# Optimization experiments

Measured on AMD Instinct MI355X. Metric: run time of the kernel, lower is better.

## Reference

```python
import jax, jax.numpy as jnp
import numpy as np

B, S, D, H, E = 4, 1024, 1024, 16, 4
HD = D // H
EPS = 1e-5


def setup_inputs() -> dict:
    key = jax.random.key(0)
    ks = jax.random.split(key, 6)
    std = 0.02
    return {
        "hidden_states": jax.random.normal(ks[0], (B, S, D), dtype=jnp.float32),
        "Wr": jax.random.normal(ks[1], (D, E), dtype=jnp.float32) * std,
        "br": jnp.zeros((E,), jnp.float32),
        "ln_g": jnp.ones((E, D), jnp.float32),
        "ln_b": jnp.zeros((E, D), jnp.float32),
        "W_attn": jax.random.normal(ks[2], (E, D, 3 * D), dtype=jnp.float32) * std,
        "b_attn": jnp.zeros((E, 3 * D), jnp.float32),
        "W_proj": jax.random.normal(ks[3], (E, D, D), dtype=jnp.float32) * std,
        "b_proj": jnp.zeros((E, D), jnp.float32),
    }


def reference(hidden_states, Wr, br, ln_g, ln_b, W_attn, b_attn, W_proj, b_proj):
    b, s, d = hidden_states.shape
    x = hidden_states.reshape(b * s, d)  # [N, D]

    # naive softmax router over experts
    score = jax.nn.softmax(x @ Wr + br, axis=-1)  # [N, E]

    # LayerNorm stats are expert-independent; affine is per-expert
    mu = jnp.mean(x, axis=-1, keepdims=True)
    var = jnp.mean(jnp.square(x - mu), axis=-1, keepdims=True)
    xn = (x - mu) * jax.lax.rsqrt(var + EPS)  # [N, D]

    ln_out = xn[:, None, :] * ln_g[None] + ln_b[None]  # [N, E, D]
    qkv_all = jnp.einsum('ned,edf->nef', ln_out, W_attn) + b_attn  # [N, E, 3D]
    # weighted_qkv: scale each expert's qkv by its routing score, sum
    qkv = jnp.einsum('ne,nef->nf', score, qkv_all)  # [N, 3D]

    q, k, v = jnp.split(qkv.reshape(b, s, 3 * d), 3, axis=-1)
    def split_heads(t):
        return t.reshape(b, s, H, HD).transpose(0, 2, 1, 3)  # [B,H,S,hd]
    q, k, v = split_heads(q), split_heads(k), split_heads(v)

    scale = 1.0 / jnp.sqrt(jnp.asarray(HD, q.dtype))
    att = jnp.einsum('bhqd,bhkd->bhqk', q, k) * scale  # [B,H,S,S]
    causal = jnp.tril(jnp.ones((s, s), dtype=bool))
    att = jnp.where(causal[None, None], att, jnp.finfo(att.dtype).min)
    probs = jax.nn.softmax(att, axis=-1)
    ctx = jnp.einsum('bhqk,bhkd->bhqd', probs, v)  # [B,H,S,hd]
    ctx = ctx.transpose(0, 2, 1, 3).reshape(b * s, d)  # [N, D]

    proj_all = jnp.einsum('nd,edf->nef', ctx, W_proj) + b_proj  # [N, E, D]
    out = jnp.einsum('ne,nef->nf', score, proj_all).reshape(b, s, d)
    return out
```

## Files before the change

### kernel.cpp

```cpp
#include <hip/hip_runtime.h>
#include <stdint.h>

#define NB 4
#define SS 1024
#define DD 1024
#define EE 4
#define HH 16
#define HDD 64
#define NN (NB*SS)
#define KK2 (EE*DD)
#define FF1 (3*DD)

typedef __attribute__((ext_vector_type(4))) float f32x4;
typedef __attribute__((ext_vector_type(8))) _Float16 half8;
typedef __attribute__((ext_vector_type(4))) _Float16 half4;

static __device__ __forceinline__ f32x4 mfma16(half8 a, half8 b, f32x4 c){
  return __builtin_amdgcn_mfma_f32_16x16x32_f16(a, b, c, 0, 0, 0);
}

#define GLOAD_LDS16(gp, lp) __builtin_amdgcn_global_load_lds( \
    (const unsigned int __attribute__((address_space(1)))*)(uintptr_t)(gp), \
    (unsigned int __attribute__((address_space(3)))*)(uintptr_t)(lp), 16, 0, 0)

#define SBAR() do { asm volatile("" ::: "memory"); \
                    __builtin_amdgcn_s_barrier(); \
                    asm volatile("" ::: "memory"); } while(0)

__device__ __forceinline__ void prep_body(
    const float* __restrict__ x, const float* __restrict__ Wr,
    const float* __restrict__ br, float* __restrict__ score,
    float* __restrict__ ratios, _Float16* __restrict__ xnb,
    int n, float (*red)[6])
{
  int tid = threadIdx.x;
  float4 xv = ((const float4*)(x + (size_t)n*DD))[tid];
  float xa[4] = {xv.x, xv.y, xv.z, xv.w};
  float vals[6];
  vals[0] = xa[0]+xa[1]+xa[2]+xa[3];
  vals[1] = xa[0]*xa[0]+xa[1]*xa[1]+xa[2]*xa[2]+xa[3]*xa[3];
  vals[2] = vals[3] = vals[4] = vals[5] = 0.f;
  #pragma unroll
  for (int j = 0; j < 4; ++j){
    float4 w = ((const float4*)Wr)[tid*4 + j];
    vals[2] += xa[j]*w.x; vals[3] += xa[j]*w.y;
    vals[4] += xa[j]*w.z; vals[5] += xa[j]*w.w;
  }
  #pragma unroll
  for (int off = 32; off >= 1; off >>= 1)
    #pragma unroll
    for (int i = 0; i < 6; ++i)
      vals[i] += __shfl_xor(vals[i], off, 64);
  int wid = tid >> 6;
  if ((tid & 63) == 0){
    #pragma unroll
    for (int i = 0; i < 6; ++i) red[wid][i] = vals[i];
  }
  __syncthreads();
  float tot[6];
  #pragma unroll
  for (int i = 0; i < 6; ++i)
    tot[i] = red[0][i] + red[1][i] + red[2][i] + red[3][i];

  float mu   = tot[0] * (1.f/DD);
  float var  = tot[1] * (1.f/DD) - mu*mu;
  float rsig = rsqrtf(var + 1e-5f);
  float lg[4];
  #pragma unroll
  for (int e = 0; e < 4; ++e) lg[e] = tot[2+e] + br[e];
  float mx = fmaxf(fmaxf(lg[0], lg[1]), fmaxf(lg[2], lg[3]));
  float ex[4], esum = 0.f;
  #pragma unroll
  for (int e = 0; e < 4; ++e){ ex[e] = __expf(lg[e] - mx); esum += ex[e]; }
  if (tid < 4){
    score[n*4 + tid] = ex[tid] / esum;
    ratios[n*4 + tid] = (tid > 0) ? (ex[tid-1] / ex[tid]) : 0.f;
  }

  half4 o;
  #pragma unroll
  for (int j = 0; j < 4; ++j) o[j] = (_Float16)((xa[j] - mu) * rsig);
  *(half4*)(xnb + (size_t)n*DD + tid*4) = o;
}

template<bool AFFINE>
__device__ __forceinline__ void transpose_body(
    const float* __restrict__ W, _Float16* __restrict__ WT, int K, int F,
    const float* __restrict__ gvec, const float* __restrict__ bvec,
    float* __restrict__ part, int k0, int f0,
    float (*t)[65], float (*red2)[64])
{
  int tid = threadIdx.x;
  int r = tid >> 4, c4 = (tid & 15) * 4;
  float pf[4] = {0.f, 0.f, 0.f, 0.f};
  #pragma unroll
  for (int i = 0; i < 4; ++i){
    int k = k0 + i*16 + r;
    float4 v = *(const float4*)(W + (size_t)k*F + f0 + c4);
    if constexpr (AFFINE){
      float bk = bvec[k];
      pf[0] += bk*v.x; pf[1] += bk*v.y; pf[2] += bk*v.z; pf[3] += bk*v.w;
      float gk = gvec[k];
      v.x *= gk; v.y *= gk; v.z *= gk; v.w *= gk;
    }
    t[i*16 + r][c4+0] = v.x; t[i*16 + r][c4+1] = v.y;
    t[i*16 + r][c4+2] = v.z; t[i*16 + r][c4+3] = v.w;
  }
  if constexpr (AFFINE){
    #pragma unroll
    for (int j = 0; j < 4; ++j) red2[r][c4+j] = pf[j];
  }
  __syncthreads();
  int f = tid >> 2, seg = tid & 3;
  half8 o0, o1;
  #pragma unroll
  for (int j = 0; j < 8; ++j){
    o0[j] = (_Float16)t[seg*16 + j][f];
    o1[j] = (_Float16)t[seg*16 + 8 + j][f];
  }
  _Float16* dst = WT + (size_t)(f0 + f)*K + k0 + seg*16;
  *(half8*)dst = o0;
  *(half8*)(dst + 8) = o1;
  if constexpr (AFFINE){
    if (tid < 64){
      float s = 0.f;
      #pragma unroll
      for (int rr = 0; rr < 16; ++rr) s += red2[rr][tid];
      part[(size_t)(k0/64) * F + f0 + tid] = s;
    }
  }
}

__global__ __launch_bounds__(256) void prep_fused_kernel(
    const float* __restrict__ W1, _Float16* __restrict__ W1T,
    const float* __restrict__ W2, _Float16* __restrict__ W2T,
    const float* __restrict__ gvec, const float* __restrict__ bvec,
    float* __restrict__ part,
    const float* __restrict__ x, const float* __restrict__ Wr,
    const float* __restrict__ br, float* __restrict__ score,
    float* __restrict__ ratios, _Float16* __restrict__ xnb)
{
  __shared__ float t[64][65];
  __shared__ float red2[16][64];
  __shared__ float red[4][6];
  int id = blockIdx.x;
  if (id & 1){
    prep_body(x, Wr, br, score, ratios, xnb, id >> 1, red);
  } else {
    int tr = id >> 1;
    int k0 = (tr & 63) * 64;
    int y  = tr >> 6;
    if (y < FF1/64)
      transpose_body<true >(W1, W1T, KK2, FF1, gvec, bvec, part, k0, y*64, t, red2);
    else
      transpose_body<false>(W2, W2T, KK2, DD, nullptr, nullptr, nullptr,
                            k0, (y - FF1/64)*64, t, red2);
  }
}

__global__ __launch_bounds__(256) void bb1_kernel(
    const float* __restrict__ b_attn, const float* __restrict__ part,
    float* __restrict__ BB1)
{
  int idx = blockIdx.x*256 + threadIdx.x;
  int e = idx / FF1, f = idx - e*FF1;
  float s = b_attn[idx];
  #pragma unroll
  for (int i = 0; i < 16; ++i)
    s += part[(size_t)(e*16 + i)*FF1 + f];
  BB1[idx] = s;
}

#define G1_BM 256
#define G1_BN 192
#define G1_BK 64
#define G1_T  (KK2/G1_BK)
#define G1_ABUF (G1_BM*G1_BK)
#define G1_BBUF (G1_BN*G1_BK)
#define G1_BUFSZ (G1_ABUF+G1_BBUF)

__global__ __launch_bounds__(512, 2) void gemm1_kernel(
    const _Float16* __restrict__ XN, const _Float16* __restrict__ BT,
    const float* __restrict__ score, const float* __restrict__ ratios,
    const float* __restrict__ bias, _Float16* __restrict__ C)
{
  __shared__ _Float16 smem[2*G1_BUFSZ];
  int tid = threadIdx.x;
  int lane = tid & 63, wid = tid >> 6;
  int q = lane & 15, g = lane >> 4;
  int wr = wid >> 1, wc = wid & 1;
  int xo = (q & 7) << 3;
  int bid = blockIdx.x;
  int xcd = bid & 7, li = bid >> 3;
  int m0 = (li >> 1) * G1_BM;
  int n0 = (xcd*2 + (li & 1)) * G1_BN;

  int arow[4], brow[6];
  #pragma unroll
  for (int mf = 0; mf < 4; ++mf) arow[mf] = (wr*64 + mf*16 + q)*64;
  #pragma unroll
  for (int nf = 0; nf < 6; ++nf) brow[nf] = G1_ABUF + (wc*96 + nf*16 + q)*64;
  int soff[2] = { (g*8) ^ xo, (32 + g*8) ^ xo };

  auto stageA = [&](int t, int buf, int h){
    const int d0 = (t & 15) * G1_BK;
    _Float16* sA = smem + buf*G1_BUFSZ;
    #pragma unroll
    for (int ld = 0; ld < 2; ++ld){
      int l = h*2 + ld;
      int c = l*512 + tid;
      int row = c >> 3;
      int seg = (c & 7) ^ (row & 7);
      GLOAD_LDS16(XN + (size_t)(m0 + row)*DD + d0 + seg*8,
                  sA + (l*512 + wid*64)*8);
    }
  };
  auto stageB = [&](int t, int buf){
    const int k0 = t * G1_BK;
    _Float16* sB = smem + buf*G1_BUFSZ + G1_ABUF;
    #pragma unroll
    for (int ld = 0; ld < 3; ++ld){
      int c = ld*512 + tid;
      int row = c >> 3;
      int seg = (c & 7) ^ (row & 7);
      GLOAD_LDS16(BT + (size_t)(n0 + row)*KK2 + k0 + seg*8,
                  sB + (ld*512 + wid*64)*8);
    }
  };

  f32x4 acc[4][6] = {};
  half8 af0[2][2], af2[2][2], bf[6][2];

  stageA(0, 0, 0); stageA(0, 0, 1); stageB(0, 0);

  for (int t = 0; t < G1_T-1; ++t){
    if (t && (t & 15) == 0){
      int e = t >> 4;
      #pragma unroll
      for (int mf = 0; mf < 4; ++mf)
        #pragma unroll
        for (int r = 0; r < 4; ++r){
          int gm = m0 + wr*64 + mf*16 + g*4 + r;
          float ratio = ratios[gm*4 + e];
          #pragma unroll
          for (int nf = 0; nf < 6; ++nf)
            acc[mf][nf][r] *= ratio;
        }
    }
    int buf = t & 1, nxt = buf ^ 1;
    const _Float16* base = smem + buf*G1_BUFSZ;
    stageA(t+1, nxt, 0);
    asm volatile("s_waitcnt vmcnt(2)" ::: "memory");
    SBAR();
    #pragma unroll
    for (int m = 0; m < 2; ++m)
      #pragma unroll
      for (int k = 0; k < 2; ++k)
        af0[m][k] = *(const half8*)(base + arow[m] + soff[k]);
    #pragma unroll
    for (int n = 0; n < 3; ++n)
      #pragma unroll
      for (int k = 0; k < 2; ++k)
        bf[n][k] = *(const half8*)(base + brow[n] + soff[k]);
    stageA(t+1, nxt, 1);
    __builtin_amdgcn_s_setprio(1);
    #pragma unroll
    for (int k = 0; k < 2; ++k)
      #pragma unroll
      for (int m = 0; m < 2; ++m)
        #pragma unroll
        for (int n = 0; n < 3; ++n)
          acc[m][n] = mfma16(af0[m][k], bf[n][k], acc[m][n]);
    __builtin_amdgcn_s_setprio(0);
    #pragma unroll
    for (int n = 3; n < 6; ++n)
      #pragma unroll
      for (int k = 0; k < 2; ++k)
        bf[n][k] = *(const half8*)(base + brow[n] + soff[k]);
    stageB(t+1, nxt);
    SBAR();
    __builtin_amdgcn_s_setprio(1);
    #pragma unroll
    for (int k = 0; k < 2; ++k)
      #pragma unroll
      for (int m = 0; m < 2; ++m)
        #pragma unroll
        for (int n = 3; n < 6; ++n)
          acc[m][n] = mfma16(af0[m][k], bf[n][k], acc[m][n]);
    __builtin_amdgcn_s_setprio(0);
    #pragma unroll
    for (int m = 0; m < 2; ++m)
      #pragma unroll
      for (int k = 0; k < 2; ++k)
        af2[m][k] = *(const half8*)(base + arow[2+m] + soff[k]);
    SBAR();
    __builtin_amdgcn_s_setprio(1);
    #pragma unroll
    for (int k = 0; k < 2; ++k)
      #pragma unroll
      for (int m = 0; m < 2; ++m)
        #pragma unroll
        for (int n = 3; n < 6; ++n)
          acc[2+m][n] = mfma16(af2[m][k], bf[n][k], acc[2+m][n]);
    #pragma unroll
    for (int k = 0; k < 2; ++k)
      #pragma unroll
      for (int m = 0; m < 2; ++m)
        #pragma unroll
        for (int n = 0; n < 3; ++n)
          acc[2+m][n] = mfma16(af2[m][k], bf[n][k], acc[2+m][n]);
    __builtin_amdgcn_s_setprio(0);
  }
  {
    const _Float16* base = smem + ((G1_T-1) & 1)*G1_BUFSZ;
    asm volatile("s_waitcnt vmcnt(0)" ::: "memory");
    SBAR();
    #pragma unroll
    for (int m = 0; m < 2; ++m)
      #pragma unroll
      for (int k = 0; k < 2; ++k){
        af0[m][k] = *(const half8*)(base + arow[m] + soff[k]);
        af2[m][k] = *(const half8*)(base + arow[2+m] + soff[k]);
      }
    #pragma unroll
    for (int n = 0; n < 6; ++n)
      #pragma unroll
      for (int k = 0; k < 2; ++k)
        bf[n][k] = *(const half8*)(base + brow[n] + soff[k]);
    #pragma unroll
    for (int k = 0; k < 2; ++k)
      #pragma unroll
      for (int m = 0; m < 2; ++m)
        #pragma unroll
        for (int n = 0; n < 6; ++n){
          acc[m][n]   = mfma16(af0[m][k], bf[n][k], acc[m][n]);
          acc[2+m][n] = mfma16(af2[m][k], bf[n][k], acc[2+m][n]);
        }
  }

  float bv[6][4];
  #pragma unroll
  for (int nf = 0; nf < 6; ++nf){
    int gn = n0 + wc*96 + nf*16 + q;
    #pragma unroll
    for (int e = 0; e < 4; ++e) bv[nf][e] = bias[e*FF1 + gn];
  }
  #pragma unroll
  for (int mf = 0; mf < 4; ++mf){
    #pragma unroll
    for (int r = 0; r < 4; ++r){
      int gm = m0 + wr*64 + mf*16 + g*4 + r;
      float4 sc = *(const float4*)(score + gm*4);
      #pragma unroll
      for (int nf = 0; nf < 6; ++nf){
        int gn = n0 + wc*96 + nf*16 + q;
        float v = acc[mf][nf][r]*sc.w
                + sc.x*bv[nf][0] + sc.y*bv[nf][1] + sc.z*bv[nf][2] + sc.w*bv[nf][3];
        C[(size_t)gm*FF1 + gn] = (_Float16)v;
      }
    }
  }
}

#define G2_BK 64
#define G2_ABUF (128*G2_BK)
#define G2_BUFSZ (2*G2_ABUF)

__global__ __launch_bounds__(512) void gemm2_kernel(
    const _Float16* __restrict__ CTX, const _Float16* __restrict__ BT,
    const float* __restrict__ score, const float* __restrict__ bias,
    float* __restrict__ Cout)
{
  __shared__ _Float16 smem[2*G2_BUFSZ];
  int tid = threadIdx.x;
  int lane = tid & 63, wid = tid >> 6;
  int q = lane & 15, g = lane >> 4;
  int wr = wid >> 2, wc = wid & 3;
  int xo = (q & 7) << 3;
  int bid = blockIdx.x;
  int xcd = bid >> 5, idx = bid & 31;
  int m0 = (xcd*4 + (idx >> 3)) * 128;
  int n0 = (idx & 7) * 128;

  int arow[4], brow[2];
  #pragma unroll
  for (int mf = 0; mf < 4; ++mf) arow[mf] = (wr*64 + mf*16 + q)*64;
  #pragma unroll
  for (int nf = 0; nf < 2; ++nf) brow[nf] = G2_ABUF + (wc*32 + nf*16 + q)*64;
  int soff[2] = { (g*8) ^ xo, (32 + g*8) ^ xo };

  auto stage = [&](int t, int buf){
    const int d0 = (t & 15) * G2_BK;
    const int k0 = t * G2_BK;
    _Float16* sA = smem + buf*G2_BUFSZ;
    _Float16* sB = sA + G2_ABUF;
    #pragma unroll
    for (int ld = 0; ld < 2; ++ld){
      int c = ld*512 + tid;
      int row = c >> 3;
      int seg = (c & 7) ^ (row & 7);
      GLOAD_LDS16(CTX + (size_t)(m0 + row)*DD + d0 + seg*8,
                  sA + (ld*512 + wid*64)*8);
    }
    #pragma unroll
    for (int ld = 0; ld < 2; ++ld){
      int c = ld*512 + tid;
      int row = c >> 3;
      int seg = (c & 7) ^ (row & 7);
      GLOAD_LDS16(BT + (size_t)(n0 + row)*KK2 + k0 + seg*8,
                  sB + (ld*512 + wid*64)*8);
    }
  };

  f32x4 accp[4][2] = {}, acco[4][2] = {};

  auto merge = [&](int e){
    #pragma unroll
    for (int m = 0; m < 4; ++m)
      #pragma unroll
      for (int r = 0; r < 4; ++r){
        int gm = m0 + wr*64 + m*16 + g*4 + r;
        float s = score[(size_t)gm*4 + e];
        #pragma unroll
        for (int n = 0; n < 2; ++n){
          acco[m][n][r] += s*accp[m][n][r];
          accp[m][n][r] = 0.f;
        }
      }
  };

  half8 af[4][2], bfr[2][2];
  auto reads = [&](const _Float16* base, int k){
    #pragma unroll
    for (int m = 0; m < 4; ++m)
      af[m][k] = *(const half8*)(base + arow[m] + soff[k]);
    #pragma unroll
    for (int n = 0; n < 2; ++n)
      bfr[n][k] = *(const half8*)(base + brow[n] + soff[k]);
  };
  auto mfmas = [&](int k){
    __builtin_amdgcn_s_setprio(1);
    #pragma unroll
    for (int m = 0; m < 4; ++m)
      #pragma unroll
      for (int n = 0; n < 2; ++n)
        accp[m][n] = mfma16(af[m][k], bfr[n][k], accp[m][n]);
    __builtin_amdgcn_s_setprio(0);
  };

  stage(0, 0);
  for (int t = 0; t < KK2/G2_BK - 1; ++t){
    const _Float16* base = smem + (t & 1)*G2_BUFSZ;
    stage(t+1, (t+1)&1);
    asm volatile("s_waitcnt vmcnt(4)" ::: "memory");
    SBAR();
    reads(base, 0);
    mfmas(0);
    reads(base, 1);
    SBAR();
    mfmas(1);
    if ((t & 15) == 15) merge(t >> 4);
  }
  {
    const _Float16* base = smem + ((KK2/G2_BK - 1) & 1)*G2_BUFSZ;
    asm volatile("s_waitcnt vmcnt(0)" ::: "memory");
    SBAR();
    reads(base, 0); reads(base, 1);
    mfmas(0); mfmas(1);
    merge(3);
  }

  #pragma unroll
  for (int m = 0; m < 4; ++m){
    #pragma unroll
    for (int r = 0; r < 4; ++r){
      int gm = m0 + wr*64 + m*16 + g*4 + r;
      float4 sc = *(const float4*)(score + gm*4);
      #pragma unroll
      for (int n = 0; n < 2; ++n){
        int gn = n0 + wc*32 + n*16 + q;
        float v = acco[m][n][r]
                + sc.x*bias[gn] + sc.y*bias[DD+gn]
                + sc.z*bias[2*DD+gn] + sc.w*bias[3*DD+gn];
        Cout[(size_t)gm*DD + gn] = v;
      }
    }
  }
}

__global__ __launch_bounds__(512) void attn_kernel(
    const _Float16* __restrict__ qkv, _Float16* __restrict__ ctx)
{
  __shared__ _Float16 lsK[2][64*64];
  __shared__ _Float16 lsV[2][64*64];
  __shared__ _Float16 lsP[8][16*64];
  int id = blockIdx.x;
  int p = id >> 1, parity = id & 1;
  int bh = p & 63;
  int qtp = p >> 6;
  int qt = parity ? qtp : 7 - qtp;
  int b = bh >> 4, h = bh & 15;
  int tid = threadIdx.x, lane = tid & 63, wid = tid >> 6;
  int q = lane & 15, g = lane >> 4;
  int xo = (q & 7) << 3;
  int qrow0 = qt*128 + wid*16;

  half8 qf[2];
  #pragma unroll
  for (int kk = 0; kk < 2; ++kk)
    qf[kk] = *(const half8*)(qkv + ((size_t)b*SS + qrow0 + q)*FF1 + h*HDD + kk*32 + g*8);

  auto issueK = [&](int kt, int buf){
    size_t kvrow = (size_t)b*SS + kt*64;
    int row = tid >> 3, seg = (tid & 7) ^ (row & 7);
    GLOAD_LDS16(qkv + (kvrow + row)*FF1 + DD + h*HDD + seg*8,
                lsK[buf] + (size_t)(wid*64)*8);
  };
  auto issueV = [&](int kt, half8& vr){
    size_t kvrow = (size_t)b*SS + kt*64;
    vr = *(const half8*)(qkv + (kvrow + lane)*FF1 + 2*DD + h*HDD + wid*8);
  };
  auto writeV = [&](half8 vr, int buf){
    #pragma unroll
    for (int j = 0; j < 8; ++j){
      int hd = wid*8 + j;
      lsV[buf][hd*64 + (lane ^ ((hd & 7) << 3))] = vr[j];
    }
  };

  f32x4 o[4] = {};
  float mrow = -1e30f, lsum = 0.f;
  const float SC2 = 0.18033688011112042f;
  int qglob = qrow0 + q;
  int ktmax = 2*qt + 1;

  half8 vr;
  issueK(0, 0);
  issueV(0, vr);

  for (int kt = 0; kt <= ktmax; ++kt){
    int cur = kt & 1, nxt = cur ^ 1;
    int tn = (kt < ktmax) ? kt+1 : ktmax;
    bool active = (kt*64 <= qrow0 + 15);
    asm volatile("s_waitcnt vmcnt(1)" ::: "memory");
    SBAR();

    f32x4 st[4] = {};
    if (active){
      __builtin_amdgcn_s_setprio(1);
      #pragma unroll
      for (int i = 0; i < 4; ++i){
        #pragma unroll
        for (int kk = 0; kk < 2; ++kk){
          half8 kf = *(const half8*)(lsK[cur] + (i*16 + q)*64 + ((kk*32 + g*8) ^ xo));
          st[i] = mfma16(kf, qf[kk], st[i]);
        }
      }
      __builtin_amdgcn_s_setprio(0);
    }
    issueK(tn, nxt);
    asm volatile("s_waitcnt vmcnt(1)" ::: "memory");
    writeV(vr, cur);

    _Float16 pb[16];
    bool resc = false;
    float psum = 0.f;
    if (active){
      float pvv[16]; float tm = -1e30f;
      if (kt*64 + 63 > qrow0){
        #pragma unroll
        for (int i = 0; i < 4; ++i)
          #pragma unroll
          for (int r = 0; r < 4; ++r){
            int kglob = kt*64 + i*16 + g*4 + r;
            float sv = (kglob <= qglob) ? st[i][r]*SC2 : -1e30f;
            pvv[i*4+r] = sv; tm = fmaxf(tm, sv);
          }
      } else {
        #pragma unroll
        for (int i = 0; i < 4; ++i)
          #pragma unroll
          for (int r = 0; r < 4; ++r){
            float sv = st[i][r]*SC2;
            pvv[i*4+r] = sv; tm = fmaxf(tm, sv);
          }
      }
      tm = fmaxf(tm, __shfl_xor(tm, 16, 64));
      tm = fmaxf(tm, __shfl_xor(tm, 32, 64));
      resc = !__all(tm <= mrow);
      float mnew = resc ? fmaxf(mrow, tm) : mrow;
      #pragma unroll
      for (int i = 0; i < 16; ++i){
        float p2 = exp2f(pvv[i] - mnew);
        psum += p2; pb[i] = (_Float16)p2;
      }
      if (resc){
        float alpha = exp2f(mrow - mnew);
        mrow = mnew;
        lsum = lsum*alpha + psum;
        float af4[4];
        #pragma unroll
        for (int r = 0; r < 4; ++r) af4[r] = __shfl(alpha, g*4 + r, 64);
        #pragma unroll
        for (int n = 0; n < 4; ++n)
          #pragma unroll
          for (int r = 0; r < 4; ++r) o[n][r] *= af4[r];
      } else {
        lsum += psum;
      }
    }
    issueV(tn, vr);

    asm volatile("s_waitcnt lgkmcnt(0)" ::: "memory");
    SBAR();

    if (active){
      #pragma unroll
      for (int i = 0; i < 4; ++i){
        half4 w4;
        w4[0]=pb[i*4+0]; w4[1]=pb[i*4+1]; w4[2]=pb[i*4+2]; w4[3]=pb[i*4+3];
        *(half4*)(&lsP[wid][q*64 + ((i*16 + g*4) ^ xo)]) = w4;
      }
      __builtin_amdgcn_s_setprio(1);
      #pragma unroll
      for (int kk = 0; kk < 2; ++kk){
        half8 pf = *(const half8*)(&lsP[wid][q*64 + ((kk*32 + g*8) ^ xo)]);
        #pragma unroll
        for (int n = 0; n < 4; ++n){
          half8 vf = *(const half8*)(&lsV[cur][(n*16 + q)*64 + ((kk*32 + g*8) ^ xo)]);
          o[n] = mfma16(pf, vf, o[n]);
        }
      }
      __builtin_amdgcn_s_setprio(0);
    }
  }
  float lt = lsum + __shfl_xor(lsum, 16, 64);
  lt = lt + __shfl_xor(lt, 32, 64);
  float rinv = 1.f / lt;
  #pragma unroll
  for (int r = 0; r < 4; ++r){
    float ri = __shfl(rinv, g*4 + r, 64);
    int qg = qt*128 + wid*16 + g*4 + r;
    _Float16* obase = ctx + ((size_t)b*SS + qg)*DD + h*HDD;
    #pragma unroll
    for (int n = 0; n < 4; ++n)
      obase[n*16 + q] = (_Float16)(o[n][r] * ri);
  }
}

extern "C" void kernel_launch(void* const* d_in, const int* in_sizes, int n_in,
                              void* d_out, int out_size, void* d_ws, size_t ws_size,
                              hipStream_t stream)
{
  const float* x      = (const float*)d_in[0];
  const float* Wr     = (const float*)d_in[1];
  const float* br     = (const float*)d_in[2];
  const float* ln_g   = (const float*)d_in[3];
  const float* ln_b   = (const float*)d_in[4];
  const float* W_attn = (const float*)d_in[5];
  const float* b_attn = (const float*)d_in[6];
  const float* W_proj = (const float*)d_in[7];
  const float* b_proj = (const float*)d_in[8];
  (void)in_sizes; (void)n_in; (void)out_size; (void)ws_size;

  char* ws = (char*)d_ws;
  size_t off = 0;
  auto alloc = [&](size_t bytes) -> void* {
    void* p = ws + off; off += (bytes + 255) & ~(size_t)255; return p;
  };
  _Float16* W1gT  = (_Float16*)alloc((size_t)FF1*KK2*2);
  _Float16* W2T   = (_Float16*)alloc((size_t)DD*KK2*2);
  float*    score = (float*)   alloc((size_t)NN*4*4);
  float*    ratio = (float*)   alloc((size_t)NN*4*4);
  _Float16* xn16  = (_Float16*)alloc((size_t)NN*DD*2);
  _Float16* qkv   = (_Float16*)alloc((size_t)NN*FF1*2);
  _Float16* ctx   = (_Float16*)alloc((size_t)NN*DD*2);
  float*    part  = (float*)   alloc((size_t)(KK2/64)*FF1*4);
  float*    BB1   = (float*)   alloc((size_t)EE*FF1*4);

  hipLaunchKernelGGL(prep_fused_kernel, dim3(8192), dim3(256), 0, stream,
                     W_attn, W1gT, W_proj, W2T, ln_g, ln_b, part,
                     x, Wr, br, score, ratio, xn16);
  hipLaunchKernelGGL(bb1_kernel, dim3(EE*FF1/256), dim3(256), 0, stream,
                     b_attn, part, BB1);
  hipLaunchKernelGGL(gemm1_kernel, dim3(256), dim3(512), 0, stream,
                     xn16, W1gT, score, ratio, BB1, qkv);
  hipLaunchKernelGGL(attn_kernel, dim3(512), dim3(512), 0, stream,
                     qkv, ctx);
  hipLaunchKernelGGL(gemm2_kernel, dim3(256), dim3(512), 0, stream,
                     ctx, W2T, score, b_proj, (float*)d_out);
}
```

Before: 201.0 us.

## Reuse normalized A tile across experts by scaling fragments with score ratios

Reorders gemm1's K loop so each 64-wide slice of the normalized input is loaded into LDS once and reused for all four experts. The A fragments held in registers are multiplied in place by cumulative score ratios (s0, then s1/s0, and so on), which removes the per-expert accumulator rescaling and the final multiply by score. B now uses a triple-buffered LDS ring, and the waitcnt/barrier schedule is rewritten around it. The cost is repeated fp16 multiplies on the A fragments, and the cumulative fp16 ratio scaling may lose accuracy or overflow/underflow when routing scores are very uneven.

```diff
diff --git a/kernel.cpp b/kernel.cpp
--- a/kernel.cpp
+++ b/kernel.cpp
@@ -26,6 +26,7 @@
 #define SBAR() do { asm volatile("" ::: "memory"); \
                     __builtin_amdgcn_s_barrier(); \
                     asm volatile("" ::: "memory"); } while(0)
+#define VMC(n) asm volatile("s_waitcnt vmcnt(" #n ")" ::: "memory")
 
 __device__ __forceinline__ void prep_body(
     const float* __restrict__ x, const float* __restrict__ Wr,
@@ -74,7 +75,7 @@
   for (int e = 0; e < 4; ++e){ ex[e] = __expf(lg[e] - mx); esum += ex[e]; }
   if (tid < 4){
     score[n*4 + tid] = ex[tid] / esum;
-    ratios[n*4 + tid] = (tid > 0) ? (ex[tid-1] / ex[tid]) : 0.f;
+    ratios[n*4 + tid] = (tid == 0) ? (ex[0] / esum) : (ex[tid] / ex[tid-1]);
   }
 
   half4 o;
@@ -174,17 +175,17 @@
 #define G1_BM 256
 #define G1_BN 192
 #define G1_BK 64
-#define G1_T  (KK2/G1_BK)
+#define G1_NT 16
 #define G1_ABUF (G1_BM*G1_BK)
 #define G1_BBUF (G1_BN*G1_BK)
-#define G1_BUFSZ (G1_ABUF+G1_BBUF)
 
 __global__ __launch_bounds__(512, 2) void gemm1_kernel(
     const _Float16* __restrict__ XN, const _Float16* __restrict__ BT,
     const float* __restrict__ score, const float* __restrict__ ratios,
     const float* __restrict__ bias, _Float16* __restrict__ C)
 {
-  __shared__ _Float16 smem[2*G1_BUFSZ];
+  __shared__ _Float16 smA[2*G1_ABUF];
+  __shared__ _Float16 smB[3*G1_BBUF];
   int tid = threadIdx.x;
   int lane = tid & 63, wid = tid >> 6;
   int q = lane & 15, g = lane >> 4;
@@ -199,25 +200,32 @@
   #pragma unroll
   for (int mf = 0; mf < 4; ++mf) arow[mf] = (wr*64 + mf*16 + q)*64;
   #pragma unroll
-  for (int nf = 0; nf < 6; ++nf) brow[nf] = G1_ABUF + (wc*96 + nf*16 + q)*64;
+  for (int nf = 0; nf < 6; ++nf) brow[nf] = (wc*96 + nf*16 + q)*64;
   int soff[2] = { (g*8) ^ xo, (32 + g*8) ^ xo };
 
-  auto stageA = [&](int t, int buf, int h){
-    const int d0 = (t & 15) * G1_BK;
-    _Float16* sA = smem + buf*G1_BUFSZ;
-    #pragma unroll
-    for (int ld = 0; ld < 2; ++ld){
-      int l = h*2 + ld;
-      int c = l*512 + tid;
+  _Float16 rf[4][4];
+  #pragma unroll
+  for (int mf = 0; mf < 4; ++mf){
+    float4 rr = *(const float4*)(ratios + (size_t)(m0 + wr*64 + mf*16 + q)*4);
+    rf[mf][0] = (_Float16)rr.x; rf[mf][1] = (_Float16)rr.y;
+    rf[mf][2] = (_Float16)rr.z; rf[mf][3] = (_Float16)rr.w;
+  }
+
+  auto stageA = [&](int t){
+    _Float16* sA = smA + (t & 1)*G1_ABUF;
+    const int d0 = t * G1_BK;
+    #pragma unroll
+    for (int ld = 0; ld < 4; ++ld){
+      int c = ld*512 + tid;
       int row = c >> 3;
       int seg = (c & 7) ^ (row & 7);
       GLOAD_LDS16(XN + (size_t)(m0 + row)*DD + d0 + seg*8,
-                  sA + (l*512 + wid*64)*8);
-    }
-  };
-  auto stageB = [&](int t, int buf){
-    const int k0 = t * G1_BK;
-    _Float16* sB = smem + buf*G1_BUFSZ + G1_ABUF;
+                  sA + (ld*512 + wid*64)*8);
+    }
+  };
+  auto stageB = [&](int gec){
+    const int k0 = (gec & 3)*DD + (gec >> 2)*G1_BK;
+    _Float16* sB = smB + (gec % 3)*G1_BBUF;
     #pragma unroll
     for (int ld = 0; ld < 3; ++ld){
       int c = ld*512 + tid;
@@ -229,113 +237,87 @@
   };
 
   f32x4 acc[4][6] = {};
-  half8 af0[2][2], af2[2][2], bf[6][2];
-
-  stageA(0, 0, 0); stageA(0, 0, 1); stageB(0, 0);
-
-  for (int t = 0; t < G1_T-1; ++t){
-    if (t && (t & 15) == 0){
-      int e = t >> 4;
-      #pragma unroll
-      for (int mf = 0; mf < 4; ++mf)
-        #pragma unroll
-        for (int r = 0; r < 4; ++r){
-          int gm = m0 + wr*64 + mf*16 + g*4 + r;
-          float ratio = ratios[gm*4 + e];
-          #pragma unroll
-          for (int nf = 0; nf < 6; ++nf)
-            acc[mf][nf][r] *= ratio;
-        }
-    }
-    int buf = t & 1, nxt = buf ^ 1;
-    const _Float16* base = smem + buf*G1_BUFSZ;
-    stageA(t+1, nxt, 0);
-    asm volatile("s_waitcnt vmcnt(2)" ::: "memory");
-    SBAR();
-    #pragma unroll
-    for (int m = 0; m < 2; ++m)
+  half8 af[4][2];
+
+  auto phase = [&](const _Float16* Ab, const _Float16* Bb,
+                   _Float16 s0, _Float16 s1, _Float16 s2, _Float16 s3,
+                   bool readAF){
+    if (readAF){
+      #pragma unroll
+      for (int m = 0; m < 4; ++m)
+        #pragma unroll
+        for (int k = 0; k < 2; ++k)
+          af[m][k] = *(const half8*)(Ab + arow[m] + soff[k]);
+    }
+    #pragma unroll
+    for (int k = 0; k < 2; ++k)
+      #pragma unroll
+      for (int j = 0; j < 8; ++j){
+        af[0][k][j] *= s0; af[1][k][j] *= s1;
+        af[2][k][j] *= s2; af[3][k][j] *= s3;
+      }
+    half8 bf[3][2];
+    #pragma unroll
+    for (int n = 0; n < 3; ++n)
       #pragma unroll
       for (int k = 0; k < 2; ++k)
-        af0[m][k] = *(const half8*)(base + arow[m] + soff[k]);
+        bf[n][k] = *(const half8*)(Bb + brow[n] + soff[k]);
+    __builtin_amdgcn_s_setprio(1);
+    #pragma unroll
+    for (int k = 0; k < 2; ++k)
+      #pragma unroll
+      for (int m = 0; m < 4; ++m)
+        #pragma unroll
+        for (int n = 0; n < 3; ++n)
+          acc[m][n] = mfma16(af[m][k], bf[n][k], acc[m][n]);
+    __builtin_amdgcn_s_setprio(0);
     #pragma unroll
     for (int n = 0; n < 3; ++n)
       #pragma unroll
       for (int k = 0; k < 2; ++k)
-        bf[n][k] = *(const half8*)(base + brow[n] + soff[k]);
-    stageA(t+1, nxt, 1);
+        bf[n][k] = *(const half8*)(Bb + brow[3+n] + soff[k]);
     __builtin_amdgcn_s_setprio(1);
     #pragma unroll
     for (int k = 0; k < 2; ++k)
       #pragma unroll
-      for (int m = 0; m < 2; ++m)
+      for (int m = 0; m < 4; ++m)
         #pragma unroll
         for (int n = 0; n < 3; ++n)
-          acc[m][n] = mfma16(af0[m][k], bf[n][k], acc[m][n]);
+          acc[m][3+n] = mfma16(af[m][k], bf[n][k], acc[m][3+n]);
     __builtin_amdgcn_s_setprio(0);
-    #pragma unroll
-    for (int n = 3; n < 6; ++n)
-      #pragma unroll
-      for (int k = 0; k < 2; ++k)
-        bf[n][k] = *(const half8*)(base + brow[n] + soff[k]);
-    stageB(t+1, nxt);
-    SBAR();
-    __builtin_amdgcn_s_setprio(1);
-    #pragma unroll
-    for (int k = 0; k < 2; ++k)
-      #pragma unroll
-      for (int m = 0; m < 2; ++m)
-        #pragma unroll
-        for (int n = 3; n < 6; ++n)
-          acc[m][n] = mfma16(af0[m][k], bf[n][k], acc[m][n]);
-    __builtin_amdgcn_s_setprio(0);
-    #pragma unroll
-    for (int m = 0; m < 2; ++m)
-      #pragma unroll
-      for (int k = 0; k < 2; ++k)
-        af2[m][k] = *(const half8*)(base + arow[2+m] + soff[k]);
-    SBAR();
-    __builtin_amdgcn_s_setprio(1);
-    #pragma unroll
-    for (int k = 0; k < 2; ++k)
-      #pragma unroll
-      for (int m = 0; m < 2; ++m)
-        #pragma unroll
-        for (int n = 3; n < 6; ++n)
-          acc[2+m][n] = mfma16(af2[m][k], bf[n][k], acc[2+m][n]);
-    #pragma unroll
-    for (int k = 0; k < 2; ++k)
-      #pragma unroll
-      for (int m = 0; m < 2; ++m)
-        #pragma unroll
-        for (int n = 0; n < 3; ++n)
-          acc[2+m][n] = mfma16(af2[m][k], bf[n][k], acc[2+m][n]);
-    __builtin_amdgcn_s_setprio(0);
+  };
+
+  stageA(0); stageB(0); stageB(1);
+
+  #pragma unroll 1
+  for (int t = 0; t < G1_NT-1; ++t){
+    const _Float16* Ab = smA + (t & 1)*G1_ABUF;
+    int g4 = t*4;
+    VMC(3); SBAR();
+    stageB(g4+2);
+    phase(Ab, smB + (g4 % 3)*G1_BBUF, rf[0][0], rf[1][0], rf[2][0], rf[3][0], true);
+    VMC(3); SBAR();
+    stageB(g4+3);
+    phase(Ab, smB + ((g4+1) % 3)*G1_BBUF, rf[0][1], rf[1][1], rf[2][1], rf[3][1], false);
+    VMC(3); SBAR();
+    stageB(g4+4); stageA(t+1);
+    phase(Ab, smB + ((g4+2) % 3)*G1_BBUF, rf[0][2], rf[1][2], rf[2][2], rf[3][2], false);
+    VMC(7); SBAR();
+    stageB(g4+5);
+    phase(Ab, smB + ((g4+3) % 3)*G1_BBUF, rf[0][3], rf[1][3], rf[2][3], rf[3][3], false);
   }
   {
-    const _Float16* base = smem + ((G1_T-1) & 1)*G1_BUFSZ;
-    asm volatile("s_waitcnt vmcnt(0)" ::: "memory");
-    SBAR();
-    #pragma unroll
-    for (int m = 0; m < 2; ++m)
-      #pragma unroll
-      for (int k = 0; k < 2; ++k){
-        af0[m][k] = *(const half8*)(base + arow[m] + soff[k]);
-        af2[m][k] = *(const half8*)(base + arow[2+m] + soff[k]);
-      }
-    #pragma unroll
-    for (int n = 0; n < 6; ++n)
-      #pragma unroll
-      for (int k = 0; k < 2; ++k)
-        bf[n][k] = *(const half8*)(base + brow[n] + soff[k]);
-    #pragma unroll
-    for (int k = 0; k < 2; ++k)
-      #pragma unroll
-      for (int m = 0; m < 2; ++m)
-        #pragma unroll
-        for (int n = 0; n < 6; ++n){
-          acc[m][n]   = mfma16(af0[m][k], bf[n][k], acc[m][n]);
-          acc[2+m][n] = mfma16(af2[m][k], bf[n][k], acc[2+m][n]);
-        }
+    const _Float16* Ab = smA + ((G1_NT-1) & 1)*G1_ABUF;
+    VMC(3); SBAR();
+    stageB(62);
+    phase(Ab, smB + (60 % 3)*G1_BBUF, rf[0][0], rf[1][0], rf[2][0], rf[3][0], true);
+    VMC(3); SBAR();
+    stageB(63);
+    phase(Ab, smB + (61 % 3)*G1_BBUF, rf[0][1], rf[1][1], rf[2][1], rf[3][1], false);
+    VMC(3); SBAR();
+    phase(Ab, smB + (62 % 3)*G1_BBUF, rf[0][2], rf[1][2], rf[2][2], rf[3][2], false);
+    VMC(0); SBAR();
+    phase(Ab, smB + (63 % 3)*G1_BBUF, rf[0][3], rf[1][3], rf[2][3], rf[3][3], false);
   }
 
   float bv[6][4];
@@ -354,7 +336,7 @@
       #pragma unroll
       for (int nf = 0; nf < 6; ++nf){
         int gn = n0 + wc*96 + nf*16 + q;
-        float v = acc[mf][nf][r]*sc.w
+        float v = acc[mf][nf][r]
                 + sc.x*bv[nf][0] + sc.y*bv[nf][1] + sc.z*bv[nf][2] + sc.w*bv[nf][3];
         C[(size_t)gm*FF1 + gn] = (_Float16)v;
       }
```

Measured after the change: 197.4 us (median of 2 runs). Within noise of the previous version (-1.8%).
